# Performance work log

Measured on AMD Instinct MI355X. Metric: run time of the kernel, lower is better.

## Reference

```python
import jax, jax.numpy as jnp
import numpy as np

BN_EPS = 1e-5


def setup_inputs() -> dict:
    key = jax.random.key(0)
    ks = jax.random.split(key, 12)
    B, C, N = 8, 256, 2048
    s = 1.0 / np.sqrt(C)
    x = jax.random.normal(ks[0], (B, C, N), dtype=jnp.float32)
    gamma = jnp.ones((C,), jnp.float32)
    beta = jnp.zeros((C,), jnp.float32)
    Wq = jax.random.normal(ks[1], (C, C), jnp.float32) * s
    bq = jnp.zeros((C,), jnp.float32)
    Wk = jax.random.normal(ks[2], (C, C), jnp.float32) * s
    bk = jnp.zeros((C,), jnp.float32)
    Wv = jax.random.normal(ks[3], (C, C), jnp.float32) * s
    bv = jnp.zeros((C,), jnp.float32)
    Wp = jax.random.normal(ks[4], (C, C), jnp.float32) * s
    bp = jnp.zeros((C,), jnp.float32)
    return {"x": x, "gamma": gamma, "beta": beta, "Wq": Wq, "bq": bq,
            "Wk": Wk, "bk": bk, "Wv": Wv, "bv": bv, "Wp": Wp, "bp": bp}


def reference(x, gamma, beta, Wq, bq, Wk, bk, Wv, bv, Wp, bp):
    B, C, N = x.shape
    # BatchNorm1d (training-mode batch stats): normalize per channel over (B, N)
    mean = jnp.mean(x, axis=(0, 2), keepdims=True)            # [1,C,1]
    var = jnp.mean(jnp.square(x - mean), axis=(0, 2), keepdims=True)
    h = (x - mean) * jax.lax.rsqrt(var + BN_EPS)
    h = h * gamma[None, :, None] + beta[None, :, None]
    # 1x1 Conv1d projections == per-position channel GEMMs
    q = jnp.einsum('oc,bcn->bno', Wq, h) + bq[None, None, :]  # [B,N,C]
    k = jnp.einsum('oc,bcn->bon', Wk, h) + bk[None, :, None]  # [B,C,N]
    v = jnp.einsum('oc,bcn->bno', Wv, h) + bv[None, None, :]  # [B,N,C]
    scale = jnp.asarray(C, x.dtype) ** -0.5
    w = jnp.einsum('bnc,bcm->bnm', q, k) * scale              # [B,N,N]
    w = jax.nn.softmax(w, axis=-1)
    h = jnp.einsum('bnm,bmc->bnc', w, v)                      # [B,N,C]
    out = jnp.einsum('oc,bnc->bon', Wp, h) + bp[None, :, None]  # [B,C,N]
    return x + out
```

## Files before the change

kernel.cpp:

```cpp
#include <hip/hip_runtime.h>
#include <hip/hip_fp16.h>

typedef _Float16 f16x8 __attribute__((ext_vector_type(8)));
typedef _Float16 f16x4 __attribute__((ext_vector_type(4)));
typedef float f32x4 __attribute__((ext_vector_type(4)));
typedef float f32x16 __attribute__((ext_vector_type(16)));

#define MFMA16(a, b, c) __builtin_amdgcn_mfma_f32_16x16x32_f16(a, b, c, 0, 0, 0)
#define MFMA32(a, b, c) __builtin_amdgcn_mfma_f32_32x32x16_f16(a, b, c, 0, 0, 0)

__device__ __forceinline__ void gload_lds16(const _Float16* g, void* l) {
    __builtin_amdgcn_global_load_lds(
        (const __attribute__((address_space(1))) void*)g,
        (__attribute__((address_space(3))) void*)l, 16, 0, 0);
}

__device__ __forceinline__ unsigned pkh(float a, float b) {
    typedef __fp16 fp16v2 __attribute__((ext_vector_type(2)));
    fp16v2 h = __builtin_amdgcn_cvt_pkrtz(a, b);
    return __builtin_bit_cast(unsigned, h);
}

__global__ __launch_bounds__(256) void prep_w_kernel(
    const float* __restrict__ Wq, const float* __restrict__ Wk,
    const float* __restrict__ Wv, const float* __restrict__ Wp,
    const float* __restrict__ bq, const float* __restrict__ bk,
    _Float16* __restrict__ out, float* __restrict__ bqk)
{
    int bid = blockIdx.x;
    int t = threadIdx.x;
    if (bid == 1024) {
        bqk[t]       = bq[t];
        bqk[256 + t] = bk[t];
        return;
    }
    int i = bid * 256 + t;
    int w = i >> 16, j = i & 65535;
    const float* src = (w == 0) ? Wq : (w == 1) ? Wk : (w == 2) ? Wv : Wp;
    out[i] = (_Float16)src[j];
}

__global__ __launch_bounds__(256) void bn_stats_kernel(
    const float* __restrict__ x, const float* __restrict__ gamma,
    const float* __restrict__ beta, float* __restrict__ scale,
    float* __restrict__ shift)
{
    int c = blockIdx.x, t = threadIdx.x;
    float s = 0.f, ss = 0.f;
    for (int b = 0; b < 8; ++b) {
        const float* p = x + ((size_t)b * 256 + c) * 2048;
        for (int n = t * 4; n < 2048; n += 1024) {
            float4 v = *(const float4*)(p + n);
            s  += v.x + v.y + v.z + v.w;
            ss += v.x*v.x + v.y*v.y + v.z*v.z + v.w*v.w;
        }
    }
    for (int off = 32; off > 0; off >>= 1) {
        s  += __shfl_down(s,  off, 64);
        ss += __shfl_down(ss, off, 64);
    }
    __shared__ float rs[4], rss[4];
    int w = t >> 6;
    if ((t & 63) == 0) { rs[w] = s; rss[w] = ss; }
    __syncthreads();
    if (t == 0) {
        float S  = rs[0] + rs[1] + rs[2] + rs[3];
        float SS = rss[0] + rss[1] + rss[2] + rss[3];
        float mean = S * (1.f / 16384.f);
        float var  = SS * (1.f / 16384.f) - mean * mean;
        float rstd = rsqrtf(var + 1e-5f);
        float sc = rstd * gamma[c];
        scale[c] = sc;
        shift[c] = beta[c] - mean * sc;
    }
}

__global__ __launch_bounds__(256) void norm_t_kernel(
    const float* __restrict__ x, const float* __restrict__ scale,
    const float* __restrict__ shift, _Float16* __restrict__ ht)
{
    __shared__ float tile[64][65];
    int t = threadIdx.x;
    int b = blockIdx.z, c0 = blockIdx.y * 64, n0 = blockIdx.x * 64;
    int nl = t & 63, cq = t >> 6;
#pragma unroll
    for (int r = 0; r < 16; ++r) {
        int cl = cq * 16 + r;
        float v = x[((size_t)b * 256 + c0 + cl) * 2048 + n0 + nl];
        tile[cl][nl] = v * scale[c0 + cl] + shift[c0 + cl];
    }
    __syncthreads();
    int cl2 = t & 63, nq = t >> 6;
#pragma unroll
    for (int r = 0; r < 16; ++r) {
        int nl2 = nq * 16 + r;
        ht[((size_t)b * 2048 + n0 + nl2) * 256 + c0 + cl2] = (_Float16)tile[cl2][nl2];
    }
}

template<typename OT, bool BIAS_I, bool RES>
__global__ __launch_bounds__(256) void gemm_nt(
    const _Float16* __restrict__ Aall, long strideA,
    const _Float16* __restrict__ Ball, long strideB,
    const float* __restrict__ bias,
    const float* __restrict__ resid, long strideR,
    OT* __restrict__ Call, long strideC,
    int M, int Nn)
{
    constexpr int K = 256;
    int b = blockIdx.z;
    const _Float16* A  = Aall + (size_t)b * strideA;
    const _Float16* Bm = Ball + (size_t)b * strideB;
    OT* C = Call + (size_t)b * strideC;
    int i0 = blockIdx.y * 128, j0 = blockIdx.x * 128;
    __shared__ _Float16 Al[128][40];
    __shared__ _Float16 Bl[128][40];
    int t = threadIdx.x, lane = t & 63, w = t >> 6;
    int lr = lane & 15, lg = lane >> 4;
    int wm = w >> 1, wn = w & 1;
    f32x4 acc[4][4] = {};
    int sr = t >> 1, sh = (t & 1) * 16;
    for (int kk = 0; kk < 8; ++kk) {
        const _Float16* ga = A  + (size_t)(i0 + sr) * K + kk * 32 + sh;
        const _Float16* gb = Bm + (size_t)(j0 + sr) * K + kk * 32 + sh;
        int4 a0 = *(const int4*)ga, a1 = *(const int4*)(ga + 8);
        int4 b0 = *(const int4*)gb, b1 = *(const int4*)(gb + 8);
        *(int4*)&Al[sr][sh] = a0; *(int4*)&Al[sr][sh + 8] = a1;
        *(int4*)&Bl[sr][sh] = b0; *(int4*)&Bl[sr][sh + 8] = b1;
        __syncthreads();
        f16x8 af[4], bf[4];
#pragma unroll
        for (int f = 0; f < 4; ++f) af[f] = *(const f16x8*)&Al[wm * 64 + f * 16 + lr][8 * lg];
#pragma unroll
        for (int f = 0; f < 4; ++f) bf[f] = *(const f16x8*)&Bl[wn * 64 + f * 16 + lr][8 * lg];
#pragma unroll
        for (int fm = 0; fm < 4; ++fm)
#pragma unroll
            for (int fn = 0; fn < 4; ++fn)
                acc[fm][fn] = MFMA16(af[fm], bf[fn], acc[fm][fn]);
        __syncthreads();
    }
#pragma unroll
    for (int fm = 0; fm < 4; ++fm)
#pragma unroll
        for (int fn = 0; fn < 4; ++fn)
#pragma unroll
            for (int rr = 0; rr < 4; ++rr) {
                int row = i0 + wm * 64 + fm * 16 + lg * 4 + rr;
                int col = j0 + wn * 64 + fn * 16 + lr;
                float vv = acc[fm][fn][rr] + (BIAS_I ? bias[row] : bias[col]);
                if (RES) vv += resid[(size_t)b * strideR + (size_t)row * Nn + col];
                C[(size_t)row * Nn + col] = (OT)vv;
            }
}

__global__ __launch_bounds__(256, 2) void attn2_kernel(
    const _Float16* __restrict__ qk, const _Float16* __restrict__ vb,
    _Float16* __restrict__ Opart, float* __restrict__ mpart,
    float* __restrict__ lpart, int nsp, int mspan)
{
    int id = blockIdx.x;
    int b = id & 7;
    int rest = id >> 3;
    int qblk = rest & 15, sp = rest >> 4;
    int m_base = sp * mspan;
    int T = mspan >> 5;

    __shared__ __align__(16) char lds[66560];

    int t = threadIdx.x, ln = t & 63, w = t >> 6;
    int col = ln & 31, hi = ln >> 5;

    const _Float16* kg = qk + (size_t)b * 1048576 + 256;
    const _Float16* vg = vb + (size_t)b * 524288;

    int koffs[4], voffs[4];
#pragma unroll
    for (int i = 0; i < 4; ++i) {
        int n = w * 4 + i;
        koffs[i] = (ln >> 1) * 512 + (ln & 1) * 8 + n * 16;
        voffs[i] = (((n & 7) * 32 + (ln >> 1)) * 2048) + ((n >> 3) * 16) + (ln & 1) * 8;
    }
    int frd = col * 32 + hi * 16;

    f16x8 qf[16];
    {
        const _Float16* qp = qk + ((size_t)b * 2048 + qblk * 128 + w * 32 + col) * 512 + hi * 8;
#pragma unroll
        for (int ks = 0; ks < 16; ++ks) {
            f16x8 v = *(const f16x8*)(qp + ks * 16);
#pragma unroll
            for (int e = 0; e < 8; ++e) v[e] = v[e] * (_Float16)0.0625f;
            qf[ks] = v;
        }
    }

    f32x16 oacc[8] = {};
    float m_run = -1e30f, l_run = 0.f;

#pragma unroll
    for (int i = 0; i < 4; ++i) {
        int n = w * 4 + i;
        gload_lds16(kg + (size_t)m_base * 512 + koffs[i], lds + n * 1024);
        gload_lds16(vg + m_base + voffs[i], lds + 16384 + n * 1024);
    }
    __syncthreads();

    int buf = 0;
    for (int tt = 0; tt < T; ++tt) {
        if (tt + 1 < T) {
            int m0 = m_base + (tt + 1) * 32;
            char* kb = lds + (buf ^ 1) * 32768;
#pragma unroll
            for (int i = 0; i < 4; ++i) {
                int n = w * 4 + i;
                gload_lds16(kg + (size_t)m0 * 512 + koffs[i], kb + n * 1024);
                gload_lds16(vg + m0 + voffs[i], kb + 16384 + n * 1024);
            }
        }
        const char* kbase = lds + buf * 32768;
        const char* vbase = kbase + 16384;

        f32x16 sacc = {};
        __builtin_amdgcn_s_setprio(1);
#pragma unroll
        for (int ks = 0; ks < 16; ++ks) {
            f16x8 kf = *(const f16x8*)(kbase + ks * 1024 + frd);
            sacc = MFMA32(kf, qf[ks], sacc);
        }
        __builtin_amdgcn_s_setprio(0);

        float rm = sacc[0];
#pragma unroll
        for (int i = 1; i < 16; ++i) rm = fmaxf(rm, sacc[i]);
        rm = fmaxf(rm, __shfl_xor(rm, 32, 64));

        if (__any(rm > m_run + 8.0f)) {
            float mnew = fmaxf(m_run, rm);
            float alpha = __expf(m_run - mnew);
            l_run *= alpha;
#pragma unroll
            for (int dt = 0; dt < 8; ++dt) oacc[dt] *= alpha;
            m_run = mnew;
        }

        float pv_[16], psum = 0.f;
#pragma unroll
        for (int i = 0; i < 16; ++i) { pv_[i] = __expf(sacc[i] - m_run); psum += pv_[i]; }
        psum += __shfl_xor(psum, 32, 64);
        l_run += psum;

        unsigned W0[2], W1[2], W2[2], W3[2];
        W0[0] = pkh(pv_[0],  pv_[1]);  W0[1] = pkh(pv_[2],  pv_[3]);
        W1[0] = pkh(pv_[4],  pv_[5]);  W1[1] = pkh(pv_[6],  pv_[7]);
        W2[0] = pkh(pv_[8],  pv_[9]);  W2[1] = pkh(pv_[10], pv_[11]);
        W3[0] = pkh(pv_[12], pv_[13]); W3[1] = pkh(pv_[14], pv_[15]);

        __builtin_amdgcn_s_setprio(1);
#pragma unroll
        for (int j = 0; j < 2; ++j) {
            unsigned A0 = j ? W2[0] : W0[0], A1 = j ? W2[1] : W0[1];
            unsigned B0 = j ? W3[0] : W1[0], B1 = j ? W3[1] : W1[1];
            unsigned s0 = hi ? A0 : B0, s1 = hi ? A1 : B1;
            unsigned r0 = __shfl_xor(s0, 32, 64), r1 = __shfl_xor(s1, 32, 64);
            union { unsigned u[4]; f16x8 v; } pf;
            pf.u[0] = hi ? r0 : A0; pf.u[1] = hi ? r1 : A1;
            pf.u[2] = hi ? B0 : r0; pf.u[3] = hi ? B1 : r1;
#pragma unroll
            for (int dt = 0; dt < 8; ++dt) {
                f16x8 vf = *(const f16x8*)(vbase + j * 8192 + dt * 1024 + frd);
                oacc[dt] = MFMA32(vf, pf.v, oacc[dt]);
            }
        }
        __builtin_amdgcn_s_setprio(0);

        __syncthreads();
        buf ^= 1;
    }

    __syncthreads();
    _Float16* tr = (_Float16*)(lds + w * 16640);
    float invl = 1.0f / l_run;
#pragma unroll
    for (int dt = 0; dt < 8; ++dt)
#pragma unroll
        for (int g = 0; g < 4; ++g) {
            f16x4 q4;
#pragma unroll
            for (int e = 0; e < 4; ++e) q4[e] = (_Float16)(oacc[dt][g * 4 + e] * invl);
            int d0 = dt * 32 + g * 8 + 4 * hi;
            *(f16x4*)(tr + col * 260 + d0) = q4;
        }
    size_t region = ((size_t)((sp * 8 + b) * 16 + qblk)) * 32768;
    int rrow = ln >> 1, h = ln & 1;
    const _Float16* srcr = tr + rrow * 260 + h * 128;
    _Float16* dstr = Opart + region + (size_t)(w * 32 + rrow) * 256 + h * 128;
#pragma unroll
    for (int i = 0; i < 16; ++i)
        *(f16x8*)(dstr + i * 8) = *(const f16x8*)(srcr + i * 8);

    if (hi == 0) {
        int qi = w * 32 + col;
        int base = ((sp * 8 + b) * 16 + qblk) * 128 + qi;
        mpart[base] = m_run;
        lpart[base] = l_run;
    }
}

__global__ __launch_bounds__(256) void combine2_kernel(
    const _Float16* __restrict__ Opart, const float* __restrict__ mpart,
    const float* __restrict__ lpart, _Float16* __restrict__ abuf, int nsp)
{
    int id = blockIdx.x;
    int b = id & 7, qb = (id >> 3) & 15, dh = id >> 7;
    int t = threadIdx.x;
    __shared__ float cf[4][128];
    if (t < 128) {
        float m[4], l[4], mx = -1e30f;
        for (int sp = 0; sp < nsp; ++sp) {
            int base = ((sp * 8 + b) * 16 + qb) * 128 + t;
            m[sp] = mpart[base]; l[sp] = lpart[base];
            mx = fmaxf(mx, m[sp]);
        }
        float Wt = 0.f;
        for (int sp = 0; sp < nsp; ++sp) {
            float wv = l[sp] * __expf(m[sp] - mx);
            cf[sp][t] = wv; Wt += wv;
        }
        float inv = 1.0f / Wt;
        for (int sp = 0; sp < nsp; ++sp) cf[sp][t] *= inv;
    }
    __syncthreads();
    size_t rb = ((size_t)(b * 16 + qb)) * 32768;
#pragma unroll
    for (int i = 0; i < 8; ++i) {
        int flat = i * 2048 + t * 8;
        int qi = flat >> 7, dl = flat & 127;
        float acc[8] = {};
        for (int sp = 0; sp < nsp; ++sp) {
            f16x8 v = *(const f16x8*)(Opart + (size_t)sp * 4194304 + rb +
                                      (size_t)qi * 256 + dh * 128 + dl);
            float c = cf[sp][qi];
#pragma unroll
            for (int e = 0; e < 8; ++e) acc[e] += c * (float)v[e];
        }
        f16x8 r;
#pragma unroll
        for (int e = 0; e < 8; ++e) r[e] = (_Float16)acc[e];
        *(f16x8*)(abuf + ((size_t)b * 2048 + qb * 128 + qi) * 256 + dh * 128 + dl) = r;
    }
}

extern "C" void kernel_launch(void* const* d_in, const int* in_sizes, int n_in,
                              void* d_out, int out_size, void* d_ws, size_t ws_size,
                              hipStream_t stream) {
    const float* x     = (const float*)d_in[0];
    const float* gamma = (const float*)d_in[1];
    const float* beta  = (const float*)d_in[2];
    const float* Wq    = (const float*)d_in[3];
    const float* bq    = (const float*)d_in[4];
    const float* Wk    = (const float*)d_in[5];
    const float* bk    = (const float*)d_in[6];
    const float* Wv    = (const float*)d_in[7];
    const float* bv    = (const float*)d_in[8];
    const float* Wp    = (const float*)d_in[9];
    const float* bp    = (const float*)d_in[10];
    float* out = (float*)d_out;

    char* ws = (char*)d_ws;
    float* scale = (float*)ws;
    float* shift = (float*)(ws + 1024);
    float* bqk   = (float*)(ws + 2048);
    float* mpart = (float*)(ws + 4096);
    float* lpart = (float*)(ws + 1052672);
    _Float16* wbf   = (_Float16*)(ws + 2101248);
    _Float16* Wvh   = wbf + 131072;
    _Float16* Wph   = wbf + 196608;
    _Float16* ht    = (_Float16*)(ws + 2625536);
    _Float16* qkbuf = (_Float16*)(ws + 11014144);
    _Float16* vbuf  = (_Float16*)(ws + 27791360);
    _Float16* Opart = (_Float16*)(ws + 36179968);
    _Float16* abuf  = ht;

    int nsp = (ws_size >= (size_t)36179968 + 4u * 8388608u) ? 4 : 2;
    int mspan = 2048 / nsp;

    const long SB = 524288;

    prep_w_kernel<<<1025, 256, 0, stream>>>(Wq, Wk, Wv, Wp, bq, bk, wbf, bqk);
    bn_stats_kernel<<<256, 256, 0, stream>>>(x, gamma, beta, scale, shift);
    norm_t_kernel<<<dim3(32, 4, 8), 256, 0, stream>>>(x, scale, shift, ht);
    gemm_nt<_Float16, false, false><<<dim3(4, 16, 8), 256, 0, stream>>>(
        ht, SB, wbf, 0, bqk, nullptr, 0, qkbuf, 1048576, 2048, 512);
    gemm_nt<_Float16, true, false><<<dim3(16, 2, 8), 256, 0, stream>>>(
        Wvh, 0, ht, SB, bv, nullptr, 0, vbuf, SB, 256, 2048);
    attn2_kernel<<<128 * nsp, 256, 0, stream>>>(qkbuf, vbuf, Opart, mpart, lpart,
                                                nsp, mspan);
    combine2_kernel<<<256, 256, 0, stream>>>(Opart, mpart, lpart, abuf, nsp);
    gemm_nt<float, true, true><<<dim3(16, 2, 8), 256, 0, stream>>>(
        Wph, 0, abuf, SB, bp, x, SB, out, SB, 256, 2048);
}
```

Measured before the change: 127.5 us.

## Double-buffer GEMM with direct-to-LDS loads and use exp2 in attention softmax

The GEMM kernel now stages A/B tiles with global_load_lds into a double-buffered LDS layout, so the next K-slice is prefetched while MFMAs run. It is templated on tile shape, and the V and output projections use 128x64 tiles for more blocks. Attention folds log2(e) into the Q scale and uses exp2, splits the QK accumulation into two chains, and tree-reduces the row max and sum. This adds LDS pressure and lowers occupancy bounds in exchange for overlap and shorter dependency chains.

```diff
diff --git a/kernel.cpp b/kernel.cpp
--- a/kernel.cpp
+++ b/kernel.cpp
@@ -19,6 +19,14 @@
     typedef __fp16 fp16v2 __attribute__((ext_vector_type(2)));
     fp16v2 h = __builtin_amdgcn_cvt_pkrtz(a, b);
     return __builtin_bit_cast(unsigned, h);
+}
+
+__device__ __forceinline__ float fexp2(float x) {
+#if __has_builtin(__builtin_amdgcn_exp2f)
+    return __builtin_amdgcn_exp2f(x);
+#else
+    return exp2f(x);
+#endif
 }
 
 __global__ __launch_bounds__(256) void prep_w_kernel(
@@ -98,56 +106,84 @@
     }
 }
 
-template<typename OT, bool BIAS_I, bool RES>
-__global__ __launch_bounds__(256) void gemm_nt(
+template<int BN, int WGM, int WGN, typename OT, bool BIAS_I, bool RES>
+__global__ __launch_bounds__(256, 3) void gemm_nt(
     const _Float16* __restrict__ Aall, long strideA,
     const _Float16* __restrict__ Ball, long strideB,
     const float* __restrict__ bias,
     const float* __restrict__ resid, long strideR,
-    OT* __restrict__ Call, long strideC,
-    int M, int Nn)
-{
-    constexpr int K = 256;
+    OT* __restrict__ Call, long strideC, int Nn)
+{
+    constexpr int BM = 128;
+    constexpr int WR = BM / WGM;
+    constexpr int WC = BN / WGN;
+    constexpr int FM = WR / 16, FN = WC / 16;
+    constexpr int BUFSZ = 8192 + BN * 64;
+    constexpr int NI = 8 + BN / 16;
+    constexpr int PW = NI / 4;
+
     int b = blockIdx.z;
     const _Float16* A  = Aall + (size_t)b * strideA;
     const _Float16* Bm = Ball + (size_t)b * strideB;
     OT* C = Call + (size_t)b * strideC;
-    int i0 = blockIdx.y * 128, j0 = blockIdx.x * 128;
-    __shared__ _Float16 Al[128][40];
-    __shared__ _Float16 Bl[128][40];
+    int i0 = blockIdx.y * BM, j0 = blockIdx.x * BN;
+
+    __shared__ __align__(16) char lds[2 * BUFSZ];
+
     int t = threadIdx.x, lane = t & 63, w = t >> 6;
     int lr = lane & 15, lg = lane >> 4;
-    int wm = w >> 1, wn = w & 1;
-    f32x4 acc[4][4] = {};
-    int sr = t >> 1, sh = (t & 1) * 16;
+    int wm = w % WGM, wn = w / WGM;
+
+    int soff = (lane >> 2) * 256 + (lane & 3) * 8;
+
+    f32x4 acc[FM][FN] = {};
+
+    auto stage = [&](int kk, int buf) {
+#pragma unroll
+        for (int i = 0; i < PW; ++i) {
+            int u = w * PW + i;
+            if (u < 8)
+                gload_lds16(A + (size_t)(i0 + u * 16) * 256 + kk * 32 + soff,
+                            lds + buf * BUFSZ + u * 1024);
+            else
+                gload_lds16(Bm + (size_t)(j0 + (u - 8) * 16) * 256 + kk * 32 + soff,
+                            lds + buf * BUFSZ + 8192 + (u - 8) * 1024);
+        }
+    };
+
+    stage(0, 0);
+    __syncthreads();
+    int buf = 0;
+#pragma unroll
     for (int kk = 0; kk < 8; ++kk) {
-        const _Float16* ga = A  + (size_t)(i0 + sr) * K + kk * 32 + sh;
-        const _Float16* gb = Bm + (size_t)(j0 + sr) * K + kk * 32 + sh;
-        int4 a0 = *(const int4*)ga, a1 = *(const int4*)(ga + 8);
-        int4 b0 = *(const int4*)gb, b1 = *(const int4*)(gb + 8);
-        *(int4*)&Al[sr][sh] = a0; *(int4*)&Al[sr][sh + 8] = a1;
-        *(int4*)&Bl[sr][sh] = b0; *(int4*)&Bl[sr][sh + 8] = b1;
+        if (kk + 1 < 8) stage(kk + 1, buf ^ 1);
+        const char* ab = lds + buf * BUFSZ;
+        const char* bb = ab + 8192;
+        f16x8 af[FM], bf[FN];
+#pragma unroll
+        for (int f = 0; f < FM; ++f)
+            af[f] = *(const f16x8*)(ab + (wm * WR + f * 16 + lr) * 64 + lg * 16);
+#pragma unroll
+        for (int f = 0; f < FN; ++f)
+            bf[f] = *(const f16x8*)(bb + (wn * WC + f * 16 + lr) * 64 + lg * 16);
+        __builtin_amdgcn_s_setprio(1);
+#pragma unroll
+        for (int fm = 0; fm < FM; ++fm)
+#pragma unroll
+            for (int fn = 0; fn < FN; ++fn)
+                acc[fm][fn] = MFMA16(af[fm], bf[fn], acc[fm][fn]);
+        __builtin_amdgcn_s_setprio(0);
         __syncthreads();
-        f16x8 af[4], bf[4];
-#pragma unroll
-        for (int f = 0; f < 4; ++f) af[f] = *(const f16x8*)&Al[wm * 64 + f * 16 + lr][8 * lg];
-#pragma unroll
-        for (int f = 0; f < 4; ++f) bf[f] = *(const f16x8*)&Bl[wn * 64 + f * 16 + lr][8 * lg];
-#pragma unroll
-        for (int fm = 0; fm < 4; ++fm)
-#pragma unroll
-            for (int fn = 0; fn < 4; ++fn)
-                acc[fm][fn] = MFMA16(af[fm], bf[fn], acc[fm][fn]);
-        __syncthreads();
-    }
-#pragma unroll
-    for (int fm = 0; fm < 4; ++fm)
-#pragma unroll
-        for (int fn = 0; fn < 4; ++fn)
+        buf ^= 1;
+    }
+#pragma unroll
+    for (int fm = 0; fm < FM; ++fm)
+#pragma unroll
+        for (int fn = 0; fn < FN; ++fn)
 #pragma unroll
             for (int rr = 0; rr < 4; ++rr) {
-                int row = i0 + wm * 64 + fm * 16 + lg * 4 + rr;
-                int col = j0 + wn * 64 + fn * 16 + lr;
+                int row = i0 + wm * WR + fm * 16 + lg * 4 + rr;
+                int col = j0 + wn * WC + fn * 16 + lr;
                 float vv = acc[fm][fn][rr] + (BIAS_I ? bias[row] : bias[col]);
                 if (RES) vv += resid[(size_t)b * strideR + (size_t)row * Nn + col];
                 C[(size_t)row * Nn + col] = (OT)vv;
@@ -190,7 +226,7 @@
         for (int ks = 0; ks < 16; ++ks) {
             f16x8 v = *(const f16x8*)(qp + ks * 16);
 #pragma unroll
-            for (int e = 0; e < 8; ++e) v[e] = v[e] * (_Float16)0.0625f;
+            for (int e = 0; e < 8; ++e) v[e] = v[e] * (_Float16)0.09016844f;
             qf[ks] = v;
         }
     }
@@ -221,32 +257,44 @@
         const char* kbase = lds + buf * 32768;
         const char* vbase = kbase + 16384;
 
-        f32x16 sacc = {};
+        f32x16 s0 = {}, s1 = {};
         __builtin_amdgcn_s_setprio(1);
 #pragma unroll
-        for (int ks = 0; ks < 16; ++ks) {
-            f16x8 kf = *(const f16x8*)(kbase + ks * 1024 + frd);
-            sacc = MFMA32(kf, qf[ks], sacc);
+        for (int ks = 0; ks < 16; ks += 2) {
+            f16x8 kf0 = *(const f16x8*)(kbase + ks * 1024 + frd);
+            f16x8 kf1 = *(const f16x8*)(kbase + (ks + 1) * 1024 + frd);
+            s0 = MFMA32(kf0, qf[ks], s0);
+            s1 = MFMA32(kf1, qf[ks + 1], s1);
         }
         __builtin_amdgcn_s_setprio(0);
-
-        float rm = sacc[0];
-#pragma unroll
-        for (int i = 1; i < 16; ++i) rm = fmaxf(rm, sacc[i]);
+        f32x16 sacc = s0 + s1;
+
+        float a0 = fmaxf(sacc[0], sacc[8]),  a1 = fmaxf(sacc[1], sacc[9]);
+        float a2 = fmaxf(sacc[2], sacc[10]), a3 = fmaxf(sacc[3], sacc[11]);
+        float a4 = fmaxf(sacc[4], sacc[12]), a5 = fmaxf(sacc[5], sacc[13]);
+        float a6 = fmaxf(sacc[6], sacc[14]), a7 = fmaxf(sacc[7], sacc[15]);
+        a0 = fmaxf(a0, a4); a1 = fmaxf(a1, a5); a2 = fmaxf(a2, a6); a3 = fmaxf(a3, a7);
+        a0 = fmaxf(a0, a2); a1 = fmaxf(a1, a3);
+        float rm = fmaxf(a0, a1);
         rm = fmaxf(rm, __shfl_xor(rm, 32, 64));
 
         if (__any(rm > m_run + 8.0f)) {
             float mnew = fmaxf(m_run, rm);
-            float alpha = __expf(m_run - mnew);
+            float alpha = fexp2(m_run - mnew);
             l_run *= alpha;
 #pragma unroll
             for (int dt = 0; dt < 8; ++dt) oacc[dt] *= alpha;
             m_run = mnew;
         }
 
-        float pv_[16], psum = 0.f;
-#pragma unroll
-        for (int i = 0; i < 16; ++i) { pv_[i] = __expf(sacc[i] - m_run); psum += pv_[i]; }
+        float pv_[16];
+#pragma unroll
+        for (int i = 0; i < 16; ++i) pv_[i] = fexp2(sacc[i] - m_run);
+        float q0s = (pv_[0] + pv_[8])  + (pv_[1] + pv_[9]);
+        float q1s = (pv_[2] + pv_[10]) + (pv_[3] + pv_[11]);
+        float q2s = (pv_[4] + pv_[12]) + (pv_[5] + pv_[13]);
+        float q3s = (pv_[6] + pv_[14]) + (pv_[7] + pv_[15]);
+        float psum = (q0s + q1s) + (q2s + q3s);
         psum += __shfl_xor(psum, 32, 64);
         l_run += psum;
 
@@ -261,8 +309,8 @@
         for (int j = 0; j < 2; ++j) {
             unsigned A0 = j ? W2[0] : W0[0], A1 = j ? W2[1] : W0[1];
             unsigned B0 = j ? W3[0] : W1[0], B1 = j ? W3[1] : W1[1];
-            unsigned s0 = hi ? A0 : B0, s1 = hi ? A1 : B1;
-            unsigned r0 = __shfl_xor(s0, 32, 64), r1 = __shfl_xor(s1, 32, 64);
+            unsigned sx0 = hi ? A0 : B0, sx1 = hi ? A1 : B1;
+            unsigned r0 = __shfl_xor(sx0, 32, 64), r1 = __shfl_xor(sx1, 32, 64);
             union { unsigned u[4]; f16x8 v; } pf;
             pf.u[0] = hi ? r0 : A0; pf.u[1] = hi ? r1 : A1;
             pf.u[2] = hi ? B0 : r0; pf.u[3] = hi ? B1 : r1;
@@ -324,7 +372,7 @@
         }
         float Wt = 0.f;
         for (int sp = 0; sp < nsp; ++sp) {
-            float wv = l[sp] * __expf(m[sp] - mx);
+            float wv = l[sp] * fexp2(m[sp] - mx);
             cf[sp][t] = wv; Wt += wv;
         }
         float inv = 1.0f / Wt;
@@ -390,13 +438,13 @@
     prep_w_kernel<<<1025, 256, 0, stream>>>(Wq, Wk, Wv, Wp, bq, bk, wbf, bqk);
     bn_stats_kernel<<<256, 256, 0, stream>>>(x, gamma, beta, scale, shift);
     norm_t_kernel<<<dim3(32, 4, 8), 256, 0, stream>>>(x, scale, shift, ht);
-    gemm_nt<_Float16, false, false><<<dim3(4, 16, 8), 256, 0, stream>>>(
-        ht, SB, wbf, 0, bqk, nullptr, 0, qkbuf, 1048576, 2048, 512);
-    gemm_nt<_Float16, true, false><<<dim3(16, 2, 8), 256, 0, stream>>>(
-        Wvh, 0, ht, SB, bv, nullptr, 0, vbuf, SB, 256, 2048);
+    gemm_nt<128, 2, 2, _Float16, false, false><<<dim3(4, 16, 8), 256, 0, stream>>>(
+        ht, SB, wbf, 0, bqk, nullptr, 0, qkbuf, 1048576, 512);
+    gemm_nt<64, 4, 1, _Float16, true, false><<<dim3(32, 2, 8), 256, 0, stream>>>(
+        Wvh, 0, ht, SB, bv, nullptr, 0, vbuf, SB, 2048);
     attn2_kernel<<<128 * nsp, 256, 0, stream>>>(qkbuf, vbuf, Opart, mpart, lpart,
                                                 nsp, mspan);
     combine2_kernel<<<256, 256, 0, stream>>>(Opart, mpart, lpart, abuf, nsp);
-    gemm_nt<float, true, true><<<dim3(16, 2, 8), 256, 0, stream>>>(
-        Wph, 0, abuf, SB, bp, x, SB, out, SB, 256, 2048);
-}
+    gemm_nt<64, 4, 1, float, true, true><<<dim3(32, 2, 8), 256, 0, stream>>>(
+        Wph, 0, abuf, SB, bp, x, SB, out, SB, 2048);
+}
```

New measurement: 112.6 us. 11.7% less time.
